# Kernel tuning notes

Measured on AMD Instinct MI355X. Metric: run time of the kernel, lower is better.

## Reference

```python
import jax, jax.numpy as jnp
import numpy as np
import math

D_MODEL = 1024
NUM_HEADS = 16
D_HEAD = 64
K_EIG = 16
B, N = 4, 4096


def setup_inputs() -> dict:
    key = jax.random.key(0)
    ks = jax.random.split(key, 8)
    s = 1.0 / math.sqrt(D_MODEL)
    return {
        "x": jax.random.normal(ks[0], (B, N, D_MODEL), jnp.float32),
        "Wq": jax.random.normal(ks[1], (D_MODEL, NUM_HEADS * D_HEAD), jnp.float32) * s,
        "bq": jnp.zeros((NUM_HEADS * D_HEAD,), jnp.float32),
        "Wk": jax.random.normal(ks[2], (D_MODEL, NUM_HEADS * D_HEAD), jnp.float32) * s,
        "bk": jnp.zeros((NUM_HEADS * D_HEAD,), jnp.float32),
        "Wv": jax.random.normal(ks[3], (D_MODEL, NUM_HEADS * D_HEAD), jnp.float32) * s,
        "bv": jnp.zeros((NUM_HEADS * D_HEAD,), jnp.float32),
        "eigenvectors": jax.random.normal(ks[4], (NUM_HEADS, K_EIG), jnp.float32),
        "filter_weights": jnp.ones((K_EIG,), jnp.float32),
    }


def reference(x, Wq, bq, Wk, bk, Wv, bv, eigenvectors, filter_weights):
    Bb, Nn, _ = x.shape
    H, Dh = NUM_HEADS, D_HEAD
    # projections -> [B,N,H,Dh]
    Q = (x @ Wq + bq).reshape(Bb, Nn, H, Dh)
    K = (x @ Wk + bk).reshape(Bb, Nn, H, Dh)
    V = (x @ Wv + bv).reshape(Bb, Nn, H, Dh)
    # head axis -> eigen (frequency) axis: [B,N,K,Dh]
    Qf = jnp.einsum('hk,bnhd->bnkd', eigenvectors, Q)
    Kf = jnp.einsum('hk,bnhd->bnkd', eigenvectors, K)
    Vf = jnp.einsum('hk,bnhd->bnkd', eigenvectors, V)
    # learnable spectral filter, broadcast over eigen axis
    w = filter_weights[None, None, :, None]
    Qf = Qf * w
    Kf = Kf * w
    Vf = Vf * w
    # small k x k attention per token
    scores = jnp.einsum('bnkd,bnld->bnkl', Qf, Kf) / math.sqrt(Dh)
    attn = jax.nn.softmax(scores, axis=-1)  # dropout is identity in eval
    out_f = jnp.einsum('bnkl,bnld->bnkd', attn, Vf)
    # back to head space: [B,N,H,Dh]
    out = jnp.einsum('hk,bnkd->bnhd', eigenvectors, out_f)
    return out.reshape(Bb, Nn, H * Dh)
```

## Files before the change

kernel.cpp:

```cpp
#include <hip/hip_runtime.h>
#include <stdint.h>

#define NTOK   16384
#define DM     1024
#define NQKV   3072

typedef __attribute__((ext_vector_type(8))) _Float16 half8;
typedef __attribute__((ext_vector_type(4))) _Float16 half4;
typedef __attribute__((ext_vector_type(4))) float    float4v;

#define MFMA16 __builtin_amdgcn_mfma_f32_16x16x32_f16
#define BARX()  do{ asm volatile("" ::: "memory"); __builtin_amdgcn_s_barrier(); asm volatile("" ::: "memory"); }while(0)
#define VMCNT(N) asm volatile("s_waitcnt vmcnt(" #N ")" ::: "memory")

__device__ __forceinline__ void async_cp16(const void* g, void* l){
  __builtin_amdgcn_global_load_lds(
      (const __attribute__((address_space(1))) void*)g,
      (__attribute__((address_space(3))) void*)l, 16, 0, 0);
}

__global__ void cvt_x_kernel(const float* __restrict__ x, _Float16* __restrict__ xb){
  int i = (blockIdx.x * blockDim.x + threadIdx.x) * 8;
  const int stride = gridDim.x * blockDim.x * 8;
  for(; i < NTOK * DM; i += stride){
    float4v v0 = *(const float4v*)(x + i);
    float4v v1 = *(const float4v*)(x + i + 4);
    half8 o;
    o[0]=(_Float16)v0[0]; o[1]=(_Float16)v0[1]; o[2]=(_Float16)v0[2]; o[3]=(_Float16)v0[3];
    o[4]=(_Float16)v1[0]; o[5]=(_Float16)v1[1]; o[6]=(_Float16)v1[2]; o[7]=(_Float16)v1[3];
    *(half8*)(xb + i) = o;
  }
}

__global__ __launch_bounds__(256)
void prep_w_kernel(const float* __restrict__ Wq, const float* __restrict__ Wk,
                   const float* __restrict__ Wv, const float* __restrict__ E,
                   const float* __restrict__ fw, _Float16* __restrict__ WT){
  __shared__ float Wl[8][1032];
  __shared__ float oT[16][8][65];
  __shared__ float sEv[256];
  __shared__ float sFw[16];
  const int t  = threadIdx.x;
  const int bx = blockIdx.x;
  const int p  = bx >> 7, rt = bx & 127;
  const int c0 = rt * 8;
  const float* W = (p == 0) ? Wq : (p == 1) ? Wk : Wv;
  sEv[t] = E[t];
  if(t < 16) sFw[t] = fw[t];

  #pragma unroll
  for(int j = 0; j < 32; ++j){
    const int flat = j * 256 + t;
    const int row = flat >> 10, col = flat & 1023;
    Wl[row][col] = W[(size_t)(c0 + row) * 1024 + col];
  }
  __syncthreads();

  const int d = t & 63, rg = t >> 6;
  #pragma unroll
  for(int rr = 0; rr < 2; ++rr){
    const int row = rg * 2 + rr;
    float w[16];
    #pragma unroll
    for(int h = 0; h < 16; ++h) w[h] = Wl[row][h * 64 + d];
    #pragma unroll
    for(int ke = 0; ke < 16; ++ke){
      float acc = 0.f;
      #pragma unroll
      for(int h = 0; h < 16; ++h) acc += sEv[h * 16 + ke] * w[h];
      oT[ke][row][d] = acc * sFw[ke];
    }
  }
  __syncthreads();

  #pragma unroll
  for(int k4 = 0; k4 < 4; ++k4){
    const int idx = k4 * 256 + t;
    const int ke = idx >> 6, dd = idx & 63;
    half8 o;
    #pragma unroll
    for(int c = 0; c < 8; ++c) o[c] = (_Float16)oT[ke][c][dd];
    const int n = (p == 2) ? (2048 + dd * 16 + ke) : (p * 1024 + ke * 64 + dd);
    *(half8*)(WT + (size_t)n * 1024 + c0) = o;
  }
}

__global__ void prep_b_kernel(const float* __restrict__ bq, const float* __restrict__ bk,
                              const float* __restrict__ bv, const float* __restrict__ E,
                              const float* __restrict__ fw, float* __restrict__ fb){
  const int n = blockIdx.x * blockDim.x + threadIdx.x;
  if(n >= NQKV) return;
  const int p = n >> 10;
  int kE, d;
  if(p == 2){ kE = n & 15; d = (n >> 4) & 63; }
  else      { kE = (n >> 6) & 15; d = n & 63; }
  const float* b = (p == 0) ? bq : (p == 1) ? bk : bv;
  float acc = 0.f;
  for(int h = 0; h < 16; ++h) acc += E[h * 16 + kE] * b[h * 64 + d];
  fb[n] = acc * fw[kE];
}

struct FlagF { static constexpr bool value = false; };
struct FlagT { static constexpr bool value = true; };

__global__ __launch_bounds__(512, 2)
void gemm_qkv_kernel(const _Float16* __restrict__ A,
                     const _Float16* __restrict__ BT,
                     const float* __restrict__ bias,
                     _Float16* __restrict__ C){
  extern __shared__ _Float16 lds[];
  const int t = threadIdx.x;
  const int lane = t & 63, wv = t >> 6;
  const int l15 = lane & 15, q = lane >> 4;
  const int wr = wv >> 2, wc = wv & 3;

  const int bid = blockIdx.x;
  const int xcd = bid & 7, s = bid >> 3;
  const int mt = xcd * 8 + (s & 7);
  const int nt = s >> 3;
  const int m0 = mt * 256, n0 = nt * 256;

  const int stR = wv * 16 + (lane >> 3);
  const int stC = (((lane & 7) ^ (lane >> 3)) * 8);
  const int stD = (wv * 128 + lane) * 8;
  const int qsw = (q * 8) ^ ((l15 & 7) * 8);
  const int aoffb = (wr * 16 + l15) * 64;
  const int boffb = (wc * 16 + l15) * 64;

  auto stgA = [&](_Float16* nb, int kc, int h){
    const _Float16* g = A + (size_t)(m0 + h * 128 + stR) * 1024 + kc + stC;
    _Float16* d = nb + h * 8192 + stD;
    async_cp16(g, d);
    async_cp16(g + 8 * 1024, d + 512);
  };
  auto stgB = [&](_Float16* nb, int kc, int h){
    const _Float16* g = BT + (size_t)(n0 + h * 128 + stR) * 1024 + kc + stC;
    _Float16* d = nb + 16384 + h * 8192 + stD;
    async_cp16(g, d);
    async_cp16(g + 8 * 1024, d + 512);
  };

  float4v acc[8][4];
  #pragma unroll
  for(int m = 0; m < 8; ++m)
    #pragma unroll
    for(int n = 0; n < 4; ++n){ acc[m][n][0]=0.f; acc[m][n][1]=0.f; acc[m][n][2]=0.f; acc[m][n][3]=0.f; }

  stgB(lds, 0, 0);
  stgB(lds, 0, 1);
  stgA(lds, 0, 0);
  stgA(lds, 0, 1);
  VMCNT(0);
  BARX();

  int kt = 0;
  auto ktile = [&](auto lastc){
    constexpr bool LAST = decltype(lastc)::value;
    const _Float16* pA = lds + (kt & 1) * 32768;
    const _Float16* pB = pA + 16384;
    _Float16* nxt = lds + ((kt + 1) & 1) * 32768;
    const int kn = (kt + 1) * 64;

    half8 a0[4], a1[4], b0[4], b1[4], ah[4];

    #pragma unroll
    for(int m = 0; m < 4; ++m) a0[m] = *(const half8*)(pA + aoffb + m * 2048 + qsw);
    #pragma unroll
    for(int n = 0; n < 4; ++n) b0[n] = *(const half8*)(pB + boffb + n * 4096 + qsw);
    if constexpr(!LAST) stgB(nxt, kn, 0);
    __builtin_amdgcn_s_setprio(1);
    #pragma unroll
    for(int m = 0; m < 4; ++m)
      #pragma unroll
      for(int n = 0; n < 4; ++n)
        acc[m][n] = MFMA16(a0[m], b0[n], acc[m][n], 0, 0, 0);
    __builtin_amdgcn_s_setprio(0);

    #pragma unroll
    for(int m = 0; m < 4; ++m) a1[m] = *(const half8*)(pA + aoffb + m * 2048 + (qsw ^ 32));
    #pragma unroll
    for(int n = 0; n < 4; ++n) b1[n] = *(const half8*)(pB + boffb + n * 4096 + (qsw ^ 32));
    if constexpr(!LAST) stgB(nxt, kn, 1);
    __builtin_amdgcn_s_setprio(1);
    #pragma unroll
    for(int m = 0; m < 4; ++m)
      #pragma unroll
      for(int n = 0; n < 4; ++n)
        acc[m][n] = MFMA16(a1[m], b1[n], acc[m][n], 0, 0, 0);
    __builtin_amdgcn_s_setprio(0);

    if constexpr(!LAST){ VMCNT(4); } else { VMCNT(0); }
    BARX();

    #pragma unroll
    for(int m = 0; m < 4; ++m) ah[m] = *(const half8*)(pA + aoffb + (m + 4) * 2048 + qsw);
    if constexpr(!LAST) stgA(nxt, kn, 0);
    __builtin_amdgcn_s_setprio(1);
    #pragma unroll
    for(int m = 0; m < 4; ++m)
      #pragma unroll
      for(int n = 0; n < 4; ++n)
        acc[m + 4][n] = MFMA16(ah[m], b0[n], acc[m + 4][n], 0, 0, 0);
    __builtin_amdgcn_s_setprio(0);

    #pragma unroll
    for(int m = 0; m < 4; ++m) ah[m] = *(const half8*)(pA + aoffb + (m + 4) * 2048 + (qsw ^ 32));
    if constexpr(!LAST) stgA(nxt, kn, 1);
    __builtin_amdgcn_s_setprio(1);
    #pragma unroll
    for(int m = 0; m < 4; ++m)
      #pragma unroll
      for(int n = 0; n < 4; ++n)
        acc[m + 4][n] = MFMA16(ah[m], b1[n], acc[m + 4][n], 0, 0, 0);
    __builtin_amdgcn_s_setprio(0);

    if constexpr(!LAST){
      VMCNT(2);
      BARX();
    }
  };

  for(kt = 0; kt < 15; ++kt) ktile(FlagF{});
  ktile(FlagT{});

  #pragma unroll
  for(int n = 0; n < 4; ++n){
    const int col = n0 + (n * 4 + wc) * 16 + l15;
    const float bs = bias[col];
    #pragma unroll
    for(int m = 0; m < 8; ++m){
      const int rbase = m0 + (m * 2 + wr) * 16 + q * 4;
      #pragma unroll
      for(int r = 0; r < 4; ++r)
        C[(size_t)(rbase + r) * NQKV + col] = (_Float16)(acc[m][n][r] + bs);
    }
  }
}

__global__ __launch_bounds__(256)
void attn_kernel(const _Float16* __restrict__ QKV,
                 const float* __restrict__ E,
                 float* __restrict__ out){
  __shared__ _Float16 pT[4][16 * 32];
  __shared__ _Float16 gT[4][16 * 32];

  const int t = threadIdx.x, lane = t & 63, wv = t >> 6;
  const int l15 = lane & 15, q = lane >> 4;

  const int tok = blockIdx.x * 4 + wv;
  const _Float16* tg = QKV + (size_t)tok * 3072;

  half8 aK0 = *(const half8*)(tg + 1024 + l15 * 64 + q * 8);
  half8 aK1 = *(const half8*)(tg + 1024 + l15 * 64 + 32 + q * 8);
  half8 bQ0 = *(const half8*)(tg + l15 * 64 + q * 8);
  half8 bQ1 = *(const half8*)(tg + l15 * 64 + 32 + q * 8);
  const _Float16* tv = tg + 2048;
  half8 vf[4];
  #pragma unroll
  for(int tt = 0; tt < 4; ++tt)
    vf[tt] = *(const half8*)(tv + (tt * 16 + l15) * 16 + (q & 1) * 8);
  half8 aE;
  if(q < 2){
    float4v e0 = *(const float4v*)(E + l15 * 16 + q * 8);
    float4v e1 = *(const float4v*)(E + l15 * 16 + q * 8 + 4);
    aE[0]=(_Float16)e0[0]; aE[1]=(_Float16)e0[1]; aE[2]=(_Float16)e0[2]; aE[3]=(_Float16)e0[3];
    aE[4]=(_Float16)e1[0]; aE[5]=(_Float16)e1[1]; aE[6]=(_Float16)e1[2]; aE[7]=(_Float16)e1[3];
  }else{
    aE[0]=(_Float16)0.f; aE[1]=(_Float16)0.f; aE[2]=(_Float16)0.f; aE[3]=(_Float16)0.f;
    aE[4]=(_Float16)0.f; aE[5]=(_Float16)0.f; aE[6]=(_Float16)0.f; aE[7]=(_Float16)0.f;
  }

  #pragma unroll
  for(int s = 0; s < 4; ++s){
    const int idx = s * 64 + lane;
    const int off = (idx >> 4) * 32 + 16 + (idx & 15);
    pT[wv][off] = (_Float16)0.f;
    gT[wv][off] = (_Float16)0.f;
  }

  float4v S; S[0]=0.f; S[1]=0.f; S[2]=0.f; S[3]=0.f;
  S = MFMA16(aK0, bQ0, S, 0, 0, 0);
  S = MFMA16(aK1, bQ1, S, 0, 0, 0);

  float v[4];
  #pragma unroll
  for(int r = 0; r < 4; ++r) v[r] = S[r] * 0.125f;
  float mx = fmaxf(fmaxf(v[0], v[1]), fmaxf(v[2], v[3]));
  mx = fmaxf(mx, __shfl_xor(mx, 16));
  mx = fmaxf(mx, __shfl_xor(mx, 32));
  float e[4];
  #pragma unroll
  for(int r = 0; r < 4; ++r) e[r] = __expf(v[r] - mx);
  float sm = (e[0] + e[1]) + (e[2] + e[3]);
  sm += __shfl_xor(sm, 16);
  sm += __shfl_xor(sm, 32);
  const float rs = 1.f / sm;

  _Float16* pw = pT[wv];
  #pragma unroll
  for(int r = 0; r < 4; ++r) pw[(q * 4 + r) * 32 + l15] = (_Float16)(e[r] * rs);
  half8 bP = *(const half8*)(pw + l15 * 32 + q * 8);

  float4v G; G[0]=0.f; G[1]=0.f; G[2]=0.f; G[3]=0.f;
  G = MFMA16(aE, bP, G, 0, 0, 0);

  _Float16* gw = gT[wv];
  #pragma unroll
  for(int r = 0; r < 4; ++r) gw[(q * 4 + r) * 32 + l15] = (_Float16)G[r];
  half8 aG = *(const half8*)(gw + l15 * 32 + q * 8);

  float* ob = out + (size_t)tok * 1024;
  #pragma unroll
  for(int tt = 0; tt < 4; ++tt){
    float4v O; O[0]=0.f; O[1]=0.f; O[2]=0.f; O[3]=0.f;
    O = MFMA16(aG, vf[tt], O, 0, 0, 0);
    #pragma unroll
    for(int r = 0; r < 4; ++r)
      ob[(q * 4 + r) * 64 + tt * 16 + l15] = O[r];
  }
}

extern "C" void kernel_launch(void* const* d_in, const int* in_sizes, int n_in,
                              void* d_out, int out_size, void* d_ws, size_t ws_size,
                              hipStream_t stream){
  const float* x  = (const float*)d_in[0];
  const float* Wq = (const float*)d_in[1];
  const float* bq = (const float*)d_in[2];
  const float* Wk = (const float*)d_in[3];
  const float* bk = (const float*)d_in[4];
  const float* Wv = (const float*)d_in[5];
  const float* bv = (const float*)d_in[6];
  const float* E  = (const float*)d_in[7];
  const float* fw = (const float*)d_in[8];
  float* out = (float*)d_out;

  char* ws = (char*)d_ws;
  _Float16* xb  = (_Float16*)ws;
  _Float16* WT  = (_Float16*)(ws + (size_t)32 * 1024 * 1024);
  float*    fb  = (float*)   (ws + (size_t)39 * 1024 * 1024);
  _Float16* QKV = (_Float16*)(ws + (size_t)40 * 1024 * 1024);

  static bool attr_done = false;
  if(!attr_done){
    hipFuncSetAttribute((const void*)gemm_qkv_kernel,
                        hipFuncAttributeMaxDynamicSharedMemorySize, 131072);
    attr_done = true;
  }

  hipLaunchKernelGGL(cvt_x_kernel, dim3(2048), dim3(256), 0, stream, x, xb);
  hipLaunchKernelGGL(prep_w_kernel, dim3(384), dim3(256), 0, stream, Wq, Wk, Wv, E, fw, WT);
  hipLaunchKernelGGL(prep_b_kernel, dim3(12), dim3(256), 0, stream, bq, bk, bv, E, fw, fb);
  hipLaunchKernelGGL(gemm_qkv_kernel, dim3(768), dim3(512), 131072, stream, xb, WT, fb, QKV);
  hipLaunchKernelGGL(attn_kernel, dim3(NTOK / 4), dim3(256), 0, stream, QKV, E, out);
}
```

Before: 283.6 us.

## Fuse fp32-to-fp16 x conversion into GEMM A-tile staging and merge prep kernels

Removes the separate cvt_x pass. The GEMM now loads fp32 x straight into registers, converts it to fp16, and writes the A tiles into LDS itself, instead of copying a pre-converted fp16 buffer with async global-to-LDS loads. The bias prep is folded into the weight prep kernel, and the GEMM is split into two launches over the two halves of M. This saves a full read and write of x plus two launches, but A-tile traffic now costs registers and VALU conversion, and each k-tile waits on stricter vmcnt(0) and lgkmcnt(0) points, which may reduce overlap.

```diff
diff --git a/kernel.cpp b/kernel.cpp
--- a/kernel.cpp
+++ b/kernel.cpp
@@ -11,6 +11,7 @@
 
 #define MFMA16 __builtin_amdgcn_mfma_f32_16x16x32_f16
 #define BARX()  do{ asm volatile("" ::: "memory"); __builtin_amdgcn_s_barrier(); asm volatile("" ::: "memory"); }while(0)
+#define LGKM0() asm volatile("s_waitcnt lgkmcnt(0)" ::: "memory")
 #define VMCNT(N) asm volatile("s_waitcnt vmcnt(" #N ")" ::: "memory")
 
 __device__ __forceinline__ void async_cp16(const void* g, void* l){
@@ -19,23 +20,13 @@
       (__attribute__((address_space(3))) void*)l, 16, 0, 0);
 }
 
-__global__ void cvt_x_kernel(const float* __restrict__ x, _Float16* __restrict__ xb){
-  int i = (blockIdx.x * blockDim.x + threadIdx.x) * 8;
-  const int stride = gridDim.x * blockDim.x * 8;
-  for(; i < NTOK * DM; i += stride){
-    float4v v0 = *(const float4v*)(x + i);
-    float4v v1 = *(const float4v*)(x + i + 4);
-    half8 o;
-    o[0]=(_Float16)v0[0]; o[1]=(_Float16)v0[1]; o[2]=(_Float16)v0[2]; o[3]=(_Float16)v0[3];
-    o[4]=(_Float16)v1[0]; o[5]=(_Float16)v1[1]; o[6]=(_Float16)v1[2]; o[7]=(_Float16)v1[3];
-    *(half8*)(xb + i) = o;
-  }
-}
-
 __global__ __launch_bounds__(256)
 void prep_w_kernel(const float* __restrict__ Wq, const float* __restrict__ Wk,
-                   const float* __restrict__ Wv, const float* __restrict__ E,
-                   const float* __restrict__ fw, _Float16* __restrict__ WT){
+                   const float* __restrict__ Wv,
+                   const float* __restrict__ bq, const float* __restrict__ bk,
+                   const float* __restrict__ bv,
+                   const float* __restrict__ E,  const float* __restrict__ fw,
+                   _Float16* __restrict__ WT,    float* __restrict__ fb){
   __shared__ float Wl[8][1032];
   __shared__ float oT[16][8][65];
   __shared__ float sEv[256];
@@ -83,31 +74,32 @@
     const int n = (p == 2) ? (2048 + dd * 16 + ke) : (p * 1024 + ke * 64 + dd);
     *(half8*)(WT + (size_t)n * 1024 + c0) = o;
   }
-}
-
-__global__ void prep_b_kernel(const float* __restrict__ bq, const float* __restrict__ bk,
-                              const float* __restrict__ bv, const float* __restrict__ E,
-                              const float* __restrict__ fw, float* __restrict__ fb){
-  const int n = blockIdx.x * blockDim.x + threadIdx.x;
-  if(n >= NQKV) return;
-  const int p = n >> 10;
-  int kE, d;
-  if(p == 2){ kE = n & 15; d = (n >> 4) & 63; }
-  else      { kE = (n >> 6) & 15; d = n & 63; }
-  const float* b = (p == 0) ? bq : (p == 1) ? bk : bv;
-  float acc = 0.f;
-  for(int h = 0; h < 16; ++h) acc += E[h * 16 + kE] * b[h * 64 + d];
-  fb[n] = acc * fw[kE];
+
+  if(rt == 0){
+    const float* b = (p == 0) ? bq : (p == 1) ? bk : bv;
+    #pragma unroll
+    for(int it = 0; it < 4; ++it){
+      const int idx = it * 256 + t;
+      const int ke = idx >> 6, dd = idx & 63;
+      float acc = 0.f;
+      #pragma unroll
+      for(int h = 0; h < 16; ++h) acc += sEv[h * 16 + ke] * b[h * 64 + dd];
+      acc *= sFw[ke];
+      const int n = (p == 2) ? (2048 + dd * 16 + ke) : (p * 1024 + ke * 64 + dd);
+      fb[n] = acc;
+    }
+  }
 }
 
 struct FlagF { static constexpr bool value = false; };
 struct FlagT { static constexpr bool value = true; };
 
 __global__ __launch_bounds__(512, 2)
-void gemm_qkv_kernel(const _Float16* __restrict__ A,
+void gemm_qkv_kernel(const float* __restrict__ X,
                      const _Float16* __restrict__ BT,
                      const float* __restrict__ bias,
-                     _Float16* __restrict__ C){
+                     _Float16* __restrict__ C,
+                     int m_base){
   extern __shared__ _Float16 lds[];
   const int t = threadIdx.x;
   const int lane = t & 63, wv = t >> 6;
@@ -116,9 +108,9 @@
 
   const int bid = blockIdx.x;
   const int xcd = bid & 7, s = bid >> 3;
-  const int mt = xcd * 8 + (s & 7);
-  const int nt = s >> 3;
-  const int m0 = mt * 256, n0 = nt * 256;
+  const int mt = xcd * 4 + (s & 3);
+  const int nt = s >> 2;
+  const int m0 = m_base + mt * 256, n0 = nt * 256;
 
   const int stR = wv * 16 + (lane >> 3);
   const int stC = (((lane & 7) ^ (lane >> 3)) * 8);
@@ -127,11 +119,30 @@
   const int aoffb = (wr * 16 + l15) * 64;
   const int boffb = (wc * 16 + l15) * 64;
 
-  auto stgA = [&](_Float16* nb, int kc, int h){
-    const _Float16* g = A + (size_t)(m0 + h * 128 + stR) * 1024 + kc + stC;
-    _Float16* d = nb + h * 8192 + stD;
-    async_cp16(g, d);
-    async_cp16(g + 8 * 1024, d + 512);
+  auto issueA = [&](int kc, float4v (&af)[2][4]){
+    #pragma unroll
+    for(int h = 0; h < 2; ++h){
+      const float* g = X + (size_t)(m0 + h * 128 + stR) * 1024 + kc + stC;
+      af[h][0] = *(const float4v*)(g);
+      af[h][1] = *(const float4v*)(g + 4);
+      af[h][2] = *(const float4v*)(g + 8 * 1024);
+      af[h][3] = *(const float4v*)(g + 8 * 1024 + 4);
+    }
+  };
+  auto writeA = [&](_Float16* nb, const float4v (&af)[2][4]){
+    #pragma unroll
+    for(int h = 0; h < 2; ++h){
+      half8 o0, o1;
+      #pragma unroll
+      for(int j = 0; j < 4; ++j){
+        o0[j]     = (_Float16)af[h][0][j];
+        o0[j + 4] = (_Float16)af[h][1][j];
+        o1[j]     = (_Float16)af[h][2][j];
+        o1[j + 4] = (_Float16)af[h][3][j];
+      }
+      *(half8*)(nb + h * 8192 + stD)       = o0;
+      *(half8*)(nb + h * 8192 + stD + 512) = o1;
+    }
   };
   auto stgB = [&](_Float16* nb, int kc, int h){
     const _Float16* g = BT + (size_t)(n0 + h * 128 + stR) * 1024 + kc + stC;
@@ -146,12 +157,17 @@
     #pragma unroll
     for(int n = 0; n < 4; ++n){ acc[m][n][0]=0.f; acc[m][n][1]=0.f; acc[m][n][2]=0.f; acc[m][n][3]=0.f; }
 
-  stgB(lds, 0, 0);
-  stgB(lds, 0, 1);
-  stgA(lds, 0, 0);
-  stgA(lds, 0, 1);
-  VMCNT(0);
-  BARX();
+  {
+    float4v af0[2][4];
+    issueA(0, af0);
+    stgB(lds, 0, 0);
+    stgB(lds, 0, 1);
+    VMCNT(4);
+    writeA(lds, af0);
+    VMCNT(0);
+    LGKM0();
+    BARX();
+  }
 
   int kt = 0;
   auto ktile = [&](auto lastc){
@@ -162,6 +178,12 @@
     const int kn = (kt + 1) * 64;
 
     half8 a0[4], a1[4], b0[4], b1[4], ah[4];
+    float4v af[2][4];
+
+    if constexpr(!LAST){
+      issueA(kn, af);
+      asm volatile("" ::: "memory");
+    }
 
     #pragma unroll
     for(int m = 0; m < 4; ++m) a0[m] = *(const half8*)(pA + aoffb + m * 2048 + qsw);
@@ -189,12 +211,13 @@
         acc[m][n] = MFMA16(a1[m], b1[n], acc[m][n], 0, 0, 0);
     __builtin_amdgcn_s_setprio(0);
 
-    if constexpr(!LAST){ VMCNT(4); } else { VMCNT(0); }
-    BARX();
+    if constexpr(!LAST){
+      VMCNT(4);
+      writeA(nxt, af);
+    }
 
     #pragma unroll
     for(int m = 0; m < 4; ++m) ah[m] = *(const half8*)(pA + aoffb + (m + 4) * 2048 + qsw);
-    if constexpr(!LAST) stgA(nxt, kn, 0);
     __builtin_amdgcn_s_setprio(1);
     #pragma unroll
     for(int m = 0; m < 4; ++m)
@@ -205,7 +228,6 @@
 
     #pragma unroll
     for(int m = 0; m < 4; ++m) ah[m] = *(const half8*)(pA + aoffb + (m + 4) * 2048 + (qsw ^ 32));
-    if constexpr(!LAST) stgA(nxt, kn, 1);
     __builtin_amdgcn_s_setprio(1);
     #pragma unroll
     for(int m = 0; m < 4; ++m)
@@ -215,7 +237,8 @@
     __builtin_amdgcn_s_setprio(0);
 
     if constexpr(!LAST){
-      VMCNT(2);
+      VMCNT(0);
+      LGKM0();
       BARX();
     }
   };
@@ -335,10 +358,9 @@
   float* out = (float*)d_out;
 
   char* ws = (char*)d_ws;
-  _Float16* xb  = (_Float16*)ws;
-  _Float16* WT  = (_Float16*)(ws + (size_t)32 * 1024 * 1024);
-  float*    fb  = (float*)   (ws + (size_t)39 * 1024 * 1024);
-  _Float16* QKV = (_Float16*)(ws + (size_t)40 * 1024 * 1024);
+  _Float16* WT  = (_Float16*)ws;
+  float*    fb  = (float*)   (ws + (size_t)6 * 1024 * 1024);
+  _Float16* QKV = (_Float16*)(ws + (size_t)8 * 1024 * 1024);
 
   static bool attr_done = false;
   if(!attr_done){
@@ -347,9 +369,11 @@
     attr_done = true;
   }
 
-  hipLaunchKernelGGL(cvt_x_kernel, dim3(2048), dim3(256), 0, stream, x, xb);
-  hipLaunchKernelGGL(prep_w_kernel, dim3(384), dim3(256), 0, stream, Wq, Wk, Wv, E, fw, WT);
-  hipLaunchKernelGGL(prep_b_kernel, dim3(12), dim3(256), 0, stream, bq, bk, bv, E, fw, fb);
-  hipLaunchKernelGGL(gemm_qkv_kernel, dim3(768), dim3(512), 131072, stream, xb, WT, fb, QKV);
+  hipLaunchKernelGGL(prep_w_kernel, dim3(384), dim3(256), 0, stream,
+                     Wq, Wk, Wv, bq, bk, bv, E, fw, WT, fb);
+  hipLaunchKernelGGL(gemm_qkv_kernel, dim3(384), dim3(512), 131072, stream,
+                     x, WT, fb, QKV, 0);
+  hipLaunchKernelGGL(gemm_qkv_kernel, dim3(384), dim3(512), 131072, stream,
+                     x, WT, fb, QKV, 8192);
   hipLaunchKernelGGL(attn_kernel, dim3(NTOK / 4), dim3(256), 0, stream, QKV, E, out);
 }
```

New measurement: 326.2 us. 1.15x slower.

## Fuse per-token attention into GEMM tail via per-band completion counters

Applied to the files above, without the earlier changes.

Removes the separate attention kernel. Each GEMM block increments an atomic counter for its 256-row band, and the last of the 12 column blocks to finish runs the per-token spectral attention for that band, reading QKV it just produced (likely still in L2). The bias prep is also folded into prep_w_kernel, which zeroes the counters, and the tile-to-block mapping now groups the 12 N-tiles of a band on one XCD. This saves two kernel launches and some QKV traffic. In exchange, only 64 blocks serialize the attention work over 32 tokens per wave each, which can leave the tail poorly parallelized.

```diff
diff --git a/kernel.cpp b/kernel.cpp
--- a/kernel.cpp
+++ b/kernel.cpp
@@ -6,7 +6,6 @@
 #define NQKV   3072
 
 typedef __attribute__((ext_vector_type(8))) _Float16 half8;
-typedef __attribute__((ext_vector_type(4))) _Float16 half4;
 typedef __attribute__((ext_vector_type(4))) float    float4v;
 
 #define MFMA16 __builtin_amdgcn_mfma_f32_16x16x32_f16
@@ -34,8 +33,12 @@
 
 __global__ __launch_bounds__(256)
 void prep_w_kernel(const float* __restrict__ Wq, const float* __restrict__ Wk,
-                   const float* __restrict__ Wv, const float* __restrict__ E,
-                   const float* __restrict__ fw, _Float16* __restrict__ WT){
+                   const float* __restrict__ Wv,
+                   const float* __restrict__ bq, const float* __restrict__ bk,
+                   const float* __restrict__ bv,
+                   const float* __restrict__ E,  const float* __restrict__ fw,
+                   _Float16* __restrict__ WT,    float* __restrict__ fb,
+                   unsigned* __restrict__ ctr){
   __shared__ float Wl[8][1032];
   __shared__ float oT[16][8][65];
   __shared__ float sEv[256];
@@ -47,6 +50,7 @@
   const float* W = (p == 0) ? Wq : (p == 1) ? Wk : Wv;
   sEv[t] = E[t];
   if(t < 16) sFw[t] = fw[t];
+  if(bx == 0 && t < 64) ctr[t] = 0u;
 
   #pragma unroll
   for(int j = 0; j < 32; ++j){
@@ -83,21 +87,21 @@
     const int n = (p == 2) ? (2048 + dd * 16 + ke) : (p * 1024 + ke * 64 + dd);
     *(half8*)(WT + (size_t)n * 1024 + c0) = o;
   }
-}
-
-__global__ void prep_b_kernel(const float* __restrict__ bq, const float* __restrict__ bk,
-                              const float* __restrict__ bv, const float* __restrict__ E,
-                              const float* __restrict__ fw, float* __restrict__ fb){
-  const int n = blockIdx.x * blockDim.x + threadIdx.x;
-  if(n >= NQKV) return;
-  const int p = n >> 10;
-  int kE, d;
-  if(p == 2){ kE = n & 15; d = (n >> 4) & 63; }
-  else      { kE = (n >> 6) & 15; d = n & 63; }
-  const float* b = (p == 0) ? bq : (p == 1) ? bk : bv;
-  float acc = 0.f;
-  for(int h = 0; h < 16; ++h) acc += E[h * 16 + kE] * b[h * 64 + d];
-  fb[n] = acc * fw[kE];
+
+  if(rt == 0){
+    const float* b = (p == 0) ? bq : (p == 1) ? bk : bv;
+    #pragma unroll
+    for(int it = 0; it < 4; ++it){
+      const int idx = it * 256 + t;
+      const int ke = idx >> 6, dd = idx & 63;
+      float acc = 0.f;
+      #pragma unroll
+      for(int h = 0; h < 16; ++h) acc += sEv[h * 16 + ke] * b[h * 64 + dd];
+      acc *= sFw[ke];
+      const int n = (p == 2) ? (2048 + dd * 16 + ke) : (p * 1024 + ke * 64 + dd);
+      fb[n] = acc;
+    }
+  }
 }
 
 struct FlagF { static constexpr bool value = false; };
@@ -107,7 +111,10 @@
 void gemm_qkv_kernel(const _Float16* __restrict__ A,
                      const _Float16* __restrict__ BT,
                      const float* __restrict__ bias,
-                     _Float16* __restrict__ C){
+                     _Float16* C,
+                     const float* __restrict__ E,
+                     float* out,
+                     unsigned* ctr){
   extern __shared__ _Float16 lds[];
   const int t = threadIdx.x;
   const int lane = t & 63, wv = t >> 6;
@@ -116,9 +123,10 @@
 
   const int bid = blockIdx.x;
   const int xcd = bid & 7, s = bid >> 3;
-  const int mt = xcd * 8 + (s & 7);
-  const int nt = s >> 3;
-  const int m0 = mt * 256, n0 = nt * 256;
+  const int mtl = s / 12;
+  const int nt  = s - mtl * 12;
+  const int band = xcd * 8 + mtl;
+  const int m0 = band * 256, n0 = nt * 256;
 
   const int stR = wv * 16 + (lane >> 3);
   const int stC = (((lane & 7) ^ (lane >> 3)) * 8);
@@ -235,30 +243,18 @@
         C[(size_t)(rbase + r) * NQKV + col] = (_Float16)(acc[m][n][r] + bs);
     }
   }
-}
-
-__global__ __launch_bounds__(256)
-void attn_kernel(const _Float16* __restrict__ QKV,
-                 const float* __restrict__ E,
-                 float* __restrict__ out){
-  __shared__ _Float16 pT[4][16 * 32];
-  __shared__ _Float16 gT[4][16 * 32];
-
-  const int t = threadIdx.x, lane = t & 63, wv = t >> 6;
-  const int l15 = lane & 15, q = lane >> 4;
-
-  const int tok = blockIdx.x * 4 + wv;
-  const _Float16* tg = QKV + (size_t)tok * 3072;
-
-  half8 aK0 = *(const half8*)(tg + 1024 + l15 * 64 + q * 8);
-  half8 aK1 = *(const half8*)(tg + 1024 + l15 * 64 + 32 + q * 8);
-  half8 bQ0 = *(const half8*)(tg + l15 * 64 + q * 8);
-  half8 bQ1 = *(const half8*)(tg + l15 * 64 + 32 + q * 8);
-  const _Float16* tv = tg + 2048;
-  half8 vf[4];
-  #pragma unroll
-  for(int tt = 0; tt < 4; ++tt)
-    vf[tt] = *(const half8*)(tv + (tt * 16 + l15) * 16 + (q & 1) * 8);
+
+  __threadfence();
+  __syncthreads();
+  volatile int* flag = (int*)lds;
+  if(t == 0){
+    unsigned old = atomicAdd(&ctr[band], 1u);
+    flag[0] = (old == 11u) ? 1 : 0;
+  }
+  __syncthreads();
+  if(!flag[0]) return;
+  __threadfence();
+
   half8 aE;
   if(q < 2){
     float4v e0 = *(const float4v*)(E + l15 * 16 + q * 8);
@@ -270,53 +266,74 @@
     aE[4]=(_Float16)0.f; aE[5]=(_Float16)0.f; aE[6]=(_Float16)0.f; aE[7]=(_Float16)0.f;
   }
 
-  #pragma unroll
-  for(int s = 0; s < 4; ++s){
-    const int idx = s * 64 + lane;
-    const int off = (idx >> 4) * 32 + 16 + (idx & 15);
-    pT[wv][off] = (_Float16)0.f;
-    gT[wv][off] = (_Float16)0.f;
-  }
-
-  float4v S; S[0]=0.f; S[1]=0.f; S[2]=0.f; S[3]=0.f;
-  S = MFMA16(aK0, bQ0, S, 0, 0, 0);
-  S = MFMA16(aK1, bQ1, S, 0, 0, 0);
-
-  float v[4];
-  #pragma unroll
-  for(int r = 0; r < 4; ++r) v[r] = S[r] * 0.125f;
-  float mx = fmaxf(fmaxf(v[0], v[1]), fmaxf(v[2], v[3]));
-  mx = fmaxf(mx, __shfl_xor(mx, 16));
-  mx = fmaxf(mx, __shfl_xor(mx, 32));
-  float e[4];
-  #pragma unroll
-  for(int r = 0; r < 4; ++r) e[r] = __expf(v[r] - mx);
-  float sm = (e[0] + e[1]) + (e[2] + e[3]);
-  sm += __shfl_xor(sm, 16);
-  sm += __shfl_xor(sm, 32);
-  const float rs = 1.f / sm;
-
-  _Float16* pw = pT[wv];
-  #pragma unroll
-  for(int r = 0; r < 4; ++r) pw[(q * 4 + r) * 32 + l15] = (_Float16)(e[r] * rs);
-  half8 bP = *(const half8*)(pw + l15 * 32 + q * 8);
-
-  float4v G; G[0]=0.f; G[1]=0.f; G[2]=0.f; G[3]=0.f;
-  G = MFMA16(aE, bP, G, 0, 0, 0);
-
-  _Float16* gw = gT[wv];
-  #pragma unroll
-  for(int r = 0; r < 4; ++r) gw[(q * 4 + r) * 32 + l15] = (_Float16)G[r];
-  half8 aG = *(const half8*)(gw + l15 * 32 + q * 8);
-
-  float* ob = out + (size_t)tok * 1024;
-  #pragma unroll
-  for(int tt = 0; tt < 4; ++tt){
-    float4v O; O[0]=0.f; O[1]=0.f; O[2]=0.f; O[3]=0.f;
-    O = MFMA16(aG, vf[tt], O, 0, 0, 0);
-    #pragma unroll
-    for(int r = 0; r < 4; ++r)
-      ob[(q * 4 + r) * 64 + tt * 16 + l15] = O[r];
+  _Float16* pT0 = lds + 64 + (wv * 2) * 512;
+  _Float16* gT0 = lds + 64 + 8192 + (wv * 2) * 512;
+  #pragma unroll
+  for(int par = 0; par < 2; ++par)
+    #pragma unroll
+    for(int s4 = 0; s4 < 4; ++s4){
+      const int idx = s4 * 64 + lane;
+      const int off = (idx >> 4) * 32 + 16 + (idx & 15);
+      pT0[par * 512 + off] = (_Float16)0.f;
+      gT0[par * 512 + off] = (_Float16)0.f;
+    }
+
+  const int tok0 = band * 256 + wv * 32;
+  #pragma unroll 2
+  for(int it = 0; it < 32; ++it){
+    const int tok = tok0 + it;
+    const _Float16* tg = C + (size_t)tok * 3072;
+    _Float16* pw = pT0 + (it & 1) * 512;
+    _Float16* gw = gT0 + (it & 1) * 512;
+
+    half8 aK0 = *(const half8*)(tg + 1024 + l15 * 64 + q * 8);
+    half8 aK1 = *(const half8*)(tg + 1024 + l15 * 64 + 32 + q * 8);
+    half8 bQ0 = *(const half8*)(tg + l15 * 64 + q * 8);
+    half8 bQ1 = *(const half8*)(tg + l15 * 64 + 32 + q * 8);
+    const _Float16* tv = tg + 2048;
+    half8 vf[4];
+    #pragma unroll
+    for(int tt = 0; tt < 4; ++tt)
+      vf[tt] = *(const half8*)(tv + (tt * 16 + l15) * 16 + (q & 1) * 8);
+
+    float4v S; S[0]=0.f; S[1]=0.f; S[2]=0.f; S[3]=0.f;
+    S = MFMA16(aK0, bQ0, S, 0, 0, 0);
+    S = MFMA16(aK1, bQ1, S, 0, 0, 0);
+
+    float v[4];
+    #pragma unroll
+    for(int r = 0; r < 4; ++r) v[r] = S[r] * 0.125f;
+    float mx = fmaxf(fmaxf(v[0], v[1]), fmaxf(v[2], v[3]));
+    mx = fmaxf(mx, __shfl_xor(mx, 16));
+    mx = fmaxf(mx, __shfl_xor(mx, 32));
+    float e[4];
+    #pragma unroll
+    for(int r = 0; r < 4; ++r) e[r] = __expf(v[r] - mx);
+    float sm = (e[0] + e[1]) + (e[2] + e[3]);
+    sm += __shfl_xor(sm, 16);
+    sm += __shfl_xor(sm, 32);
+    const float rs = 1.f / sm;
+
+    #pragma unroll
+    for(int r = 0; r < 4; ++r) pw[(q * 4 + r) * 32 + l15] = (_Float16)(e[r] * rs);
+    half8 bP = *(const half8*)(pw + l15 * 32 + q * 8);
+
+    float4v G; G[0]=0.f; G[1]=0.f; G[2]=0.f; G[3]=0.f;
+    G = MFMA16(aE, bP, G, 0, 0, 0);
+
+    #pragma unroll
+    for(int r = 0; r < 4; ++r) gw[(q * 4 + r) * 32 + l15] = (_Float16)G[r];
+    half8 aG = *(const half8*)(gw + l15 * 32 + q * 8);
+
+    float* ob = out + (size_t)tok * 1024;
+    #pragma unroll
+    for(int tt = 0; tt < 4; ++tt){
+      float4v O; O[0]=0.f; O[1]=0.f; O[2]=0.f; O[3]=0.f;
+      O = MFMA16(aG, vf[tt], O, 0, 0, 0);
+      #pragma unroll
+      for(int r = 0; r < 4; ++r)
+        ob[(q * 4 + r) * 64 + tt * 16 + l15] = O[r];
+    }
   }
 }
 
@@ -337,7 +354,8 @@
   char* ws = (char*)d_ws;
   _Float16* xb  = (_Float16*)ws;
   _Float16* WT  = (_Float16*)(ws + (size_t)32 * 1024 * 1024);
-  float*    fb  = (float*)   (ws + (size_t)39 * 1024 * 1024);
+  float*    fb  = (float*)   (ws + (size_t)38 * 1024 * 1024);
+  unsigned* ctr = (unsigned*)(ws + (size_t)39 * 1024 * 1024);
   _Float16* QKV = (_Float16*)(ws + (size_t)40 * 1024 * 1024);
 
   static bool attr_done = false;
@@ -348,8 +366,8 @@
   }
 
   hipLaunchKernelGGL(cvt_x_kernel, dim3(2048), dim3(256), 0, stream, x, xb);
-  hipLaunchKernelGGL(prep_w_kernel, dim3(384), dim3(256), 0, stream, Wq, Wk, Wv, E, fw, WT);
-  hipLaunchKernelGGL(prep_b_kernel, dim3(12), dim3(256), 0, stream, bq, bk, bv, E, fw, fb);
-  hipLaunchKernelGGL(gemm_qkv_kernel, dim3(768), dim3(512), 131072, stream, xb, WT, fb, QKV);
-  hipLaunchKernelGGL(attn_kernel, dim3(NTOK / 4), dim3(256), 0, stream, QKV, E, out);
-}
+  hipLaunchKernelGGL(prep_w_kernel, dim3(384), dim3(256), 0, stream,
+                     Wq, Wk, Wv, bq, bk, bv, E, fw, WT, fb, ctr);
+  hipLaunchKernelGGL(gemm_qkv_kernel, dim3(768), dim3(512), 131072, stream,
+                     xb, WT, fb, QKV, E, out, ctr);
+}
```

Result: slower. 607.7 us (+114.3%).
